# Optimization experiments

Measured on AMD Instinct MI355X. Metric: run time of the kernel, lower is better.

## Reference

```python
import jax, jax.numpy as jnp
import numpy as np

# Grid / physics constants (match init_kwargs)
NX, NY, NZ = 256, 256, 128
LX, LY, LZ = 1.0, 1.0, 1.0
CP, CV, MU, KTH, G = 1004.0, 717.0, 1.8e-5, 0.025, 9.8
DX = LX / NX            # periodic spacing in x
DY = LY / NY            # periodic spacing in y
DZ = LZ / (NZ - 1)      # non-periodic spacing in z


def _d1p(f, axis, d):
    # second-order central first derivative, periodic axis
    return (jnp.roll(f, -1, axis) - jnp.roll(f, 1, axis)) * (0.5 / d)


def _d2p(f, axis, d):
    # second-order central second derivative, periodic axis
    return (jnp.roll(f, -1, axis) + jnp.roll(f, 1, axis) - 2.0 * f) * (1.0 / (d * d))


def _d1z(f, d):
    # non-periodic first derivative along last axis: central interior, 2nd-order one-sided at walls
    inv2d = 0.5 / d
    c = (f[..., 2:] - f[..., :-2]) * inv2d
    lo = (-3.0 * f[..., 0:1] + 4.0 * f[..., 1:2] - f[..., 2:3]) * inv2d
    hi = (3.0 * f[..., -1:] - 4.0 * f[..., -2:-1] + f[..., -3:-2]) * inv2d
    return jnp.concatenate([lo, c, hi], axis=-1)


def _d2z(f, d):
    # non-periodic second derivative along last axis: central interior, 2nd-order one-sided at walls
    invd2 = 1.0 / (d * d)
    c = (f[..., 2:] - 2.0 * f[..., 1:-1] + f[..., :-2]) * invd2
    lo = (2.0 * f[..., 0:1] - 5.0 * f[..., 1:2] + 4.0 * f[..., 2:3] - f[..., 3:4]) * invd2
    hi = (2.0 * f[..., -1:] - 5.0 * f[..., -2:-1] + 4.0 * f[..., -3:-2] - f[..., -4:-3]) * invd2
    return jnp.concatenate([lo, c, hi], axis=-1)


def _lap(f):
    return _d2p(f, 0, DX) + _d2p(f, 1, DY) + _d2z(f, DZ)


def _adv(q, u, v, w):
    # u*dq/dx + v*dq/dy + w*dq/dz
    return u * _d1p(q, 0, DX) + v * _d1p(q, 1, DY) + w * _d1z(q, DZ)


def setup_inputs() -> dict:
    key = jax.random.key(0)
    state = 0.05 * jax.random.normal(key, (6, NX, NY, NZ), dtype=jnp.float32)
    # keep density positive and temperature physical (state order: u,v,w,rou,T,c)
    state = state.at[3].add(1.0)
    state = state.at[4].add(300.0)
    return {"state": state, "t": 0}


def reference(state, t):
    u, v, w, rou, T, c = state  # each [NX, NY, NZ]
    p = (CP - CV) * rou * T

    # NOTE: original code only applies -d/dx(rou*u) to drou; the y/z flux line is a no-op expression.
    drou = -_d1p(rou * u, 0, DX)

    du = (-_d1p(p, 0, DX) + MU * _lap(u)) / rou - _adv(u, u, v, w)
    dv = (-_d1p(p, 1, DY) + MU * _lap(v)) / rou - _adv(v, u, v, w)
    dw = (-G * rou - _d1z(p, DZ) + MU * _lap(w)) / rou - _adv(w, u, v, w)
    dT = KTH * _lap(T) / rou / CV - _adv(T, u, v, w)
    dc = -_adv(c, u, v, w)

    result = jnp.stack([du, dv, dw, drou, dT, dc], axis=0)
    # zero momentum and temperature tendencies at z walls
    result = result.at[0:3, :, :, 0].set(0.0)
    result = result.at[0:3, :, :, -1].set(0.0)
    result = result.at[4, :, :, 0].set(0.0)
    result = result.at[4, :, :, -1].set(0.0)
    return result
```

## Files before the change

### kernel.cpp

```cpp
#include <hip/hip_runtime.h>


namespace {
constexpr int NXc = 256, NYc = 256, NZc = 128;
constexpr int FS = NXc * NYc * NZc;
constexpr int XS = NYc * NZc;
constexpr int YS = NZc;

constexpr float MUc = 1.8e-5f, KTHc = 0.025f, Gc = 9.8f;
constexpr float Rgas = 287.0f;
constexpr float invCV = 1.0f / 717.0f;

constexpr float inv2dx = 128.0f, inv2dy = 128.0f, inv2dz = 63.5f;
constexpr float invdx2 = 65536.0f, invdy2 = 65536.0f, invdz2 = 16129.0f;

typedef float nf4 __attribute__((ext_vector_type(4)));
}

__device__ __forceinline__ float4 ld4(const float* __restrict__ p, int i4) {
    return reinterpret_cast<const float4*>(p)[i4];
}

__device__ __forceinline__ void st_nt(float4 v, float4* p) {
    nf4 nv;
    nv.x = v.x; nv.y = v.y; nv.z = v.z; nv.w = v.w;
    __builtin_nontemporal_store(nv, reinterpret_cast<nf4*>(p));
}

#define LOADN(q, sq) \
    const float4 q##_xm = ld4(sq, bxm4), q##_xp = ld4(sq, bxp4); \
    const float4 q##_ym = ld4(sq, bym4), q##_yp = ld4(sq, byp4); \
    const float q##_zm = __shfl_up(q##_c.w, 1, 32); \
    const float q##_zp = __shfl_down(q##_c.x, 1, 32);

#define ADV_LAP_C(q, C, PREV, NEXT) \
    adv_##q.C = u_c.C * (q##_xp.C - q##_xm.C) * inv2dx \
              + v_c.C * (q##_yp.C - q##_ym.C) * inv2dy \
              + w_c.C * ((NEXT) - (PREV)) * inv2dz; \
    lap_##q.C = (q##_xp.C + q##_xm.C - 2.0f * q##_c.C) * invdx2 \
              + (q##_yp.C + q##_ym.C - 2.0f * q##_c.C) * invdy2 \
              + ((NEXT) + (PREV) - 2.0f * q##_c.C) * invdz2;

#define DERIVS(q) \
    float4 adv_##q, lap_##q; \
    ADV_LAP_C(q, x, q##_zm,  q##_c.y) \
    ADV_LAP_C(q, y, q##_c.x, q##_c.z) \
    ADV_LAP_C(q, z, q##_c.y, q##_c.w) \
    ADV_LAP_C(q, w, q##_c.z, q##_zp)

__global__ __launch_bounds__(256) void rb_kernel(const float* __restrict__ s,
                                                 float* __restrict__ o) {
    const int l = threadIdx.x;
    const int y = blockIdx.x * 8 + threadIdx.y;
    const int x = blockIdx.y;

    const int xm = (x == 0) ? NXc - 1 : x - 1;
    const int xp = (x == NXc - 1) ? 0 : x + 1;
    const int ym = (y == 0) ? NYc - 1 : y - 1;
    const int yp = (y == NYc - 1) ? 0 : y + 1;

    const int b4   = (x * XS + y * YS) / 4 + l;
    const int bxm4 = (xm * XS + y * YS) / 4 + l;
    const int bxp4 = (xp * XS + y * YS) / 4 + l;
    const int bym4 = (x * XS + ym * YS) / 4 + l;
    const int byp4 = (x * XS + yp * YS) / 4 + l;

    const float* su = s;
    const float* sv = s + FS;
    const float* sw = s + 2 * FS;
    const float* sr = s + 3 * FS;
    const float* st = s + 4 * FS;
    const float* sc = s + 5 * FS;

    const float4 u_c = ld4(su, b4), v_c = ld4(sv, b4), w_c = ld4(sw, b4);
    const float4 r_c = ld4(sr, b4), T_c = ld4(st, b4), c_c = ld4(sc, b4);

    float4 inv_r;
    inv_r.x = 1.0f / r_c.x; inv_r.y = 1.0f / r_c.y;
    inv_r.z = 1.0f / r_c.z; inv_r.w = 1.0f / r_c.w;

    LOADN(T, st)
    DERIVS(T)
    LOADN(r, sr)

    float4 p_c, p_xm, p_xp, p_ym, p_yp;
#define PC(C) \
    p_c.C  = Rgas * r_c.C  * T_c.C; \
    p_xm.C = Rgas * r_xm.C * T_xm.C;  p_xp.C = Rgas * r_xp.C * T_xp.C; \
    p_ym.C = Rgas * r_ym.C * T_ym.C;  p_yp.C = Rgas * r_yp.C * T_yp.C;
    PC(x) PC(y) PC(z) PC(w)
#undef PC
    const float p_zm = __shfl_up(p_c.w, 1, 32);
    const float p_zp = __shfl_down(p_c.x, 1, 32);

    float4 dpdx, dpdy, dpdz;
#define DP(C) \
    dpdx.C = (p_xp.C - p_xm.C) * inv2dx; \
    dpdy.C = (p_yp.C - p_ym.C) * inv2dy;
    DP(x) DP(y) DP(z) DP(w)
#undef DP
    dpdz.x = (p_c.y - p_zm) * inv2dz;
    dpdz.y = (p_c.z - p_c.x) * inv2dz;
    dpdz.z = (p_c.w - p_c.y) * inv2dz;
    dpdz.w = (p_zp  - p_c.z) * inv2dz;

    LOADN(u, su)
    DERIVS(u)
    float4 drou;
#define DR(C) drou.C = -(r_xp.C * u_xp.C - r_xm.C * u_xm.C) * inv2dx;
    DR(x) DR(y) DR(z) DR(w)
#undef DR

    LOADN(v, sv)
    DERIVS(v)

    LOADN(w, sw)
    DERIVS(w)

    LOADN(c, sc)
    DERIVS(c)
    (void)lap_c;

    float4 du4, dv4, dw4, dT4, dc4;
#define OUT(C) \
    du4.C = (-dpdx.C + MUc * lap_u.C) * inv_r.C - adv_u.C; \
    dv4.C = (-dpdy.C + MUc * lap_v.C) * inv_r.C - adv_v.C; \
    dw4.C = (-Gc * r_c.C - dpdz.C + MUc * lap_w.C) * inv_r.C - adv_w.C; \
    dT4.C = KTHc * lap_T.C * inv_r.C * invCV - adv_T.C; \
    dc4.C = -adv_c.C;
    OUT(x) OUT(y) OUT(z) OUT(w)
#undef OUT

    if (l == 0) {
        du4.x = 0.0f; dv4.x = 0.0f; dw4.x = 0.0f; dT4.x = 0.0f;
        const float dzc0 = (-3.0f * c_c.x + 4.0f * c_c.y - c_c.z) * inv2dz;
        dc4.x = -(u_c.x * (c_xp.x - c_xm.x) * inv2dx
                + v_c.x * (c_yp.x - c_ym.x) * inv2dy
                + w_c.x * dzc0);
    }
    if (l == 31) {
        du4.w = 0.0f; dv4.w = 0.0f; dw4.w = 0.0f; dT4.w = 0.0f;
        const float dzcN = (3.0f * c_c.w - 4.0f * c_c.z + c_c.y) * inv2dz;
        dc4.w = -(u_c.w * (c_xp.w - c_xm.w) * inv2dx
                + v_c.w * (c_yp.w - c_ym.w) * inv2dy
                + w_c.w * dzcN);
    }

    float4* o4 = reinterpret_cast<float4*>(o);
    const int fs4 = FS / 4;
    st_nt(du4,  o4 + b4);
    st_nt(dv4,  o4 + b4 + fs4);
    st_nt(dw4,  o4 + b4 + 2 * fs4);
    st_nt(drou, o4 + b4 + 3 * fs4);
    st_nt(dT4,  o4 + b4 + 4 * fs4);
    st_nt(dc4,  o4 + b4 + 5 * fs4);
}

extern "C" void kernel_launch(void* const* d_in, const int* in_sizes, int n_in,
                              void* d_out, int out_size, void* d_ws, size_t ws_size,
                              hipStream_t stream) {
    (void)in_sizes; (void)n_in; (void)d_ws; (void)ws_size; (void)out_size;
    const float* s = (const float*)d_in[0];
    float* o = (float*)d_out;

    dim3 block(32, 8, 1);
    dim3 grid(NYc / 8, NXc, 1);
    rb_kernel<<<grid, block, 0, stream>>>(s, o);
}
```

Baseline: 343.7 us.

## Stage neighbor rows in LDS via async global_load_lds with smaller blocks

Each block now copies all the rows it needs (y-halo, x-1 and x+1 planes, for all six fields) into LDS using __builtin_amdgcn_global_load_lds, then reads the center and neighbor values from LDS instead of issuing separate global float4 loads. The block shrinks to 32x4 threads and the grid grows to match. This removes duplicate y-neighbor global loads within a block and uses the direct global-to-LDS path. In exchange it adds a barrier, LDS pressure of about 43KB per block, and y-halo overhead that is larger relative to the smaller block.

```diff
diff --git a/kernel.cpp b/kernel.cpp
--- a/kernel.cpp
+++ b/kernel.cpp
@@ -14,11 +14,15 @@
 constexpr float inv2dx = 128.0f, inv2dy = 128.0f, inv2dz = 63.5f;
 constexpr float invdx2 = 65536.0f, invdy2 = 65536.0f, invdz2 = 16129.0f;
 
+constexpr int BY = 4;
+constexpr int RPF = BY + 2 + BY + BY;
+constexpr int TOT_ROWS = 6 * RPF;
+constexpr int ROW_B = NZc * 4;
+constexpr int LDS_B = TOT_ROWS * ROW_B;
+
 typedef float nf4 __attribute__((ext_vector_type(4)));
-}
-
-__device__ __forceinline__ float4 ld4(const float* __restrict__ p, int i4) {
-    return reinterpret_cast<const float4*>(p)[i4];
+typedef const __attribute__((address_space(1))) unsigned int gu32;
+typedef __attribute__((address_space(3))) unsigned int lu32;
 }
 
 __device__ __forceinline__ void st_nt(float4 v, float4* p) {
@@ -27,9 +31,10 @@
     __builtin_nontemporal_store(nv, reinterpret_cast<nf4*>(p));
 }
 
-#define LOADN(q, sq) \
-    const float4 q##_xm = ld4(sq, bxm4), q##_xp = ld4(sq, bxp4); \
-    const float4 q##_ym = ld4(sq, bym4), q##_yp = ld4(sq, byp4); \
+#define LROW(fi, rr) (*(const float4*)(smem + ((fi) * RPF + (rr)) * ROW_B + tx * 16))
+#define LOADN(q, fi) \
+    const float4 q##_ym = LROW(fi, ty), q##_yp = LROW(fi, 2 + ty); \
+    const float4 q##_xm = LROW(fi, 6 + ty), q##_xp = LROW(fi, 10 + ty); \
     const float q##_zm = __shfl_up(q##_c.w, 1, 32); \
     const float q##_zp = __shfl_down(q##_c.x, 1, 32);
 
@@ -48,40 +53,50 @@
     ADV_LAP_C(q, z, q##_c.y, q##_c.w) \
     ADV_LAP_C(q, w, q##_c.z, q##_zp)
 
-__global__ __launch_bounds__(256) void rb_kernel(const float* __restrict__ s,
+__global__ __launch_bounds__(128) void rb_kernel(const float* __restrict__ s,
                                                  float* __restrict__ o) {
-    const int l = threadIdx.x;
-    const int y = blockIdx.x * 8 + threadIdx.y;
+    extern __shared__ char smem[];
+
+    const int tx = threadIdx.x;
+    const int ty = threadIdx.y;
+    const int ty0 = blockIdx.x * BY;
+    const int y = ty0 + ty;
     const int x = blockIdx.y;
 
     const int xm = (x == 0) ? NXc - 1 : x - 1;
     const int xp = (x == NXc - 1) ? 0 : x + 1;
-    const int ym = (y == 0) ? NYc - 1 : y - 1;
-    const int yp = (y == NYc - 1) ? 0 : y + 1;
 
-    const int b4   = (x * XS + y * YS) / 4 + l;
-    const int bxm4 = (xm * XS + y * YS) / 4 + l;
-    const int bxp4 = (xp * XS + y * YS) / 4 + l;
-    const int bym4 = (x * XS + ym * YS) / 4 + l;
-    const int byp4 = (x * XS + yp * YS) / 4 + l;
+    {
+        const int wid = ty >> 1;
+        const int half = ty & 1;
+        const char* sb = (const char*)s;
+        for (int p = wid; p < TOT_ROWS / 2; p += 2) {
+            const int R = 2 * p + half;
+            const int f = R / RPF;
+            const int rr = R - f * RPF;
+            int gx, gy;
+            if (rr < BY + 2)      { gx = x;  gy = (ty0 + rr + NYc - 1) & (NYc - 1); }
+            else if (rr < 2 * BY + 2) { gx = xm; gy = ty0 + (rr - (BY + 2)); }
+            else                  { gx = xp; gy = ty0 + (rr - (2 * BY + 2)); }
+            const char* gp = sb + 4u * ((unsigned)f * FS + (unsigned)gx * XS
+                                        + (unsigned)gy * YS) + tx * 16;
+            __builtin_amdgcn_global_load_lds((gu32*)gp,
+                                             (lu32*)(smem + p * 1024),
+                                             16, 0, 0);
+        }
+    }
+    __syncthreads();
 
-    const float* su = s;
-    const float* sv = s + FS;
-    const float* sw = s + 2 * FS;
-    const float* sr = s + 3 * FS;
-    const float* st = s + 4 * FS;
-    const float* sc = s + 5 * FS;
-
-    const float4 u_c = ld4(su, b4), v_c = ld4(sv, b4), w_c = ld4(sw, b4);
-    const float4 r_c = ld4(sr, b4), T_c = ld4(st, b4), c_c = ld4(sc, b4);
+    const float4 u_c = LROW(0, 1 + ty), v_c = LROW(1, 1 + ty), w_c = LROW(2, 1 + ty);
+    const float4 r_c = LROW(3, 1 + ty), T_c = LROW(4, 1 + ty), c_c = LROW(5, 1 + ty);
 
     float4 inv_r;
     inv_r.x = 1.0f / r_c.x; inv_r.y = 1.0f / r_c.y;
     inv_r.z = 1.0f / r_c.z; inv_r.w = 1.0f / r_c.w;
 
-    LOADN(T, st)
+    LOADN(T, 4)
     DERIVS(T)
-    LOADN(r, sr)
+    LOADN(r, 3)
 
     float4 p_c, p_xm, p_xp, p_ym, p_yp;
 #define PC(C) \
@@ -104,20 +119,20 @@
     dpdz.z = (p_c.w - p_c.y) * inv2dz;
     dpdz.w = (p_zp  - p_c.z) * inv2dz;
 
-    LOADN(u, su)
+    LOADN(u, 0)
     DERIVS(u)
     float4 drou;
 #define DR(C) drou.C = -(r_xp.C * u_xp.C - r_xm.C * u_xm.C) * inv2dx;
     DR(x) DR(y) DR(z) DR(w)
 #undef DR
 
-    LOADN(v, sv)
+    LOADN(v, 1)
     DERIVS(v)
 
-    LOADN(w, sw)
+    LOADN(w, 2)
     DERIVS(w)
 
-    LOADN(c, sc)
+    LOADN(c, 5)
     DERIVS(c)
     (void)lap_c;
 
@@ -131,14 +146,14 @@
     OUT(x) OUT(y) OUT(z) OUT(w)
 #undef OUT
 
-    if (l == 0) {
+    if (tx == 0) {
         du4.x = 0.0f; dv4.x = 0.0f; dw4.x = 0.0f; dT4.x = 0.0f;
         const float dzc0 = (-3.0f * c_c.x + 4.0f * c_c.y - c_c.z) * inv2dz;
         dc4.x = -(u_c.x * (c_xp.x - c_xm.x) * inv2dx
                 + v_c.x * (c_yp.x - c_ym.x) * inv2dy
                 + w_c.x * dzc0);
     }
-    if (l == 31) {
+    if (tx == 31) {
         du4.w = 0.0f; dv4.w = 0.0f; dw4.w = 0.0f; dT4.w = 0.0f;
         const float dzcN = (3.0f * c_c.w - 4.0f * c_c.z + c_c.y) * inv2dz;
         dc4.w = -(u_c.w * (c_xp.w - c_xm.w) * inv2dx
@@ -146,6 +161,7 @@
                 + w_c.w * dzcN);
     }
 
+    const int b4 = (x * XS + y * YS) / 4 + tx;
     float4* o4 = reinterpret_cast<float4*>(o);
     const int fs4 = FS / 4;
     st_nt(du4,  o4 + b4);
@@ -163,7 +179,7 @@
     const float* s = (const float*)d_in[0];
     float* o = (float*)d_out;
 
-    dim3 block(32, 8, 1);
-    dim3 grid(NYc / 8, NXc, 1);
-    rb_kernel<<<grid, block, 0, stream>>>(s, o);
+    dim3 block(32, BY, 1);
+    dim3 grid(NYc / BY, NXc, 1);
+    rb_kernel<<<grid, block, LDS_B, stream>>>(s, o);
 }
```

New measurement: 365.4 us. +6.3%, slower.
